# Performance work log

Measured on AMD Instinct MI355X. Metric: run time of the kernel, lower is better.

Reference implementation:

```python
import jax, jax.numpy as jnp
import numpy as np

SR = 44100.0
MIN_GAIN, MAX_GAIN = -48.0, 12.0
MIN_EQ, MAX_EQ = -15.0, 15.0
MIN_CTS, MAX_CTS = -20.0, 10.0
# Freeverb (JUCE Reverb, as used by pedalboard.Reverb) tunings @ 44.1 kHz
COMB_T = [1116, 1188, 1277, 1356, 1422, 1491, 1557, 1617]
AP_T = [556, 441, 341, 225]
COMB_OFF = [0]
for _L in COMB_T:
    COMB_OFF.append(COMB_OFF[-1] + _L)
AP_OFF = [0]
for _L in AP_T:
    AP_OFF.append(AP_OFF[-1] + _L)


def restore(x, lo, hi):
    # inverse of normalize-to-(0,1)
    return x * (hi - lo) + lo


def first_order(fc, kind):
    # bilinear-transform 1st-order HP/LP (pedalboard High/LowpassFilter are 1st order)
    K = jnp.tan(np.pi * fc / SR)
    a1 = (K - 1.0) / (K + 1.0)
    z = jnp.zeros_like(fc)
    if kind == "hp":
        b0 = 1.0 / (1.0 + K)
        b = jnp.stack([b0, -b0, z], -1)
    else:
        b0 = K / (1.0 + K)
        b = jnp.stack([b0, b0, z], -1)
    a = jnp.stack([jnp.ones_like(fc), a1, z], -1)
    return b, a


def shelf(fc, gain_db, high):
    # RBJ cookbook shelf, Q = 1/sqrt(2)
    A = 10.0 ** (gain_db / 40.0)
    w = 2.0 * np.pi * fc / SR
    cw = jnp.cos(w)
    alpha = jnp.sin(w) * (np.sqrt(2.0) / 2.0)
    sq = 2.0 * jnp.sqrt(A) * alpha
    s = 1.0 if high else -1.0
    b0 = A * ((A + 1.0) + s * (A - 1.0) * cw + sq)
    b1 = -2.0 * s * A * ((A - 1.0) + s * (A + 1.0) * cw)
    b2 = A * ((A + 1.0) + s * (A - 1.0) * cw - sq)
    a0 = (A + 1.0) - s * (A - 1.0) * cw + sq
    a1 = 2.0 * s * ((A - 1.0) - s * (A + 1.0) * cw)
    a2 = (A + 1.0) - s * (A - 1.0) * cw - sq
    return jnp.stack([b0, b1, b2], -1), jnp.stack([a0, a1, a2], -1)


def peak(fc, gain_db, q):
    # RBJ cookbook peaking EQ
    A = 10.0 ** (gain_db / 40.0)
    w = 2.0 * np.pi * fc / SR
    cw = jnp.cos(w)
    alpha = jnp.sin(w) / (2.0 * q)
    b = jnp.stack([1.0 + alpha * A, -2.0 * cw, 1.0 - alpha * A], -1)
    a = jnp.stack([1.0 + alpha / A, -2.0 * cw, 1.0 - alpha / A], -1)
    return b, a


def cascade_biquads(x, B, A):
    # x: [N, T]; B, A: [N, 6, 3]. DF2T cascade of 6 sections via one scan.
    B = B / A[..., :1]
    A = A / A[..., :1]
    n_sec = B.shape[1]

    def step(z, xt):  # z: [N, 6, 2], xt: [N]
        s = xt
        zn = []
        for k in range(n_sec):
            y = B[:, k, 0] * s + z[:, k, 0]
            z1 = B[:, k, 1] * s - A[:, k, 1] * y + z[:, k, 1]
            z2 = B[:, k, 2] * s - A[:, k, 2] * y
            zn.append(jnp.stack([z1, z2], -1))
            s = y
        return jnp.stack(zn, 1), s

    z0 = jnp.zeros((x.shape[0], n_sec, 2), x.dtype)
    _, y = jax.lax.scan(step, z0, x.T)
    return y.T


def compressor(x, thr_db, ratio, att_ms, rel_ms):
    # feed-forward compressor, dB-domain gain computer + one-pole attack/release
    a_att = jnp.exp(-1.0 / (att_ms * 1e-3 * SR))  # [N]
    a_rel = jnp.exp(-1.0 / (rel_ms * 1e-3 * SR))
    lvl = 20.0 * jnp.log10(jnp.abs(x) + 1e-6)  # [N, T]
    tgt = jnp.minimum(0.0, (thr_db[:, None] - lvl) * (1.0 - 1.0 / ratio[:, None]))

    def step(g, t):  # g, t: [N] gain reduction in dB (<= 0)
        coef = jnp.where(t < g, a_att, a_rel)
        g = coef * g + (1.0 - coef) * t
        return g, g

    _, g = jax.lax.scan(step, jnp.zeros(x.shape[0], x.dtype), tgt.T)
    return x * 10.0 ** (g.T / 20.0)


def freeverb(x, room, damp01, wet, dry, width):
    # JUCE/Freeverb mono: 8 parallel damped combs -> 4 series allpasses
    fb = room * 0.28 + 0.7
    damp = damp01 * 0.4
    wet1 = 3.0 * wet * 0.5 * (1.0 + width)
    dryg = 2.0 * dry
    N = x.shape[0]
    CL, AL = COMB_OFF[-1], AP_OFF[-1]

    def step(carry, xt):
        cb, ab, st, t = carry
        inp = xt * 0.015
        acc = jnp.zeros_like(xt)
        st_new = []
        for k in range(8):
            idx = COMB_OFF[k] + t % COMB_T[k]
            out = cb[:, idx]
            s = out * (1.0 - damp) + st[:, k] * damp
            cb = cb.at[:, idx].set(inp + s * fb)
            st_new.append(s)
            acc = acc + out
        for k in range(4):
            idx = AP_OFF[k] + t % AP_T[k]
            buf = ab[:, idx]
            ab = ab.at[:, idx].set(acc + buf * 0.5)
            acc = buf - acc
        y = acc * wet1 + xt * dryg
        return (cb, ab, jnp.stack(st_new, 1), t + 1), y

    carry0 = (jnp.zeros((N, CL), x.dtype), jnp.zeros((N, AL), x.dtype),
              jnp.zeros((N, 8), x.dtype), jnp.int32(0))
    _, y = jax.lax.scan(step, carry0, x.T)
    return y.T


def _forward(x, p):
    bs, nt, T = x.shape
    N = bs * nt
    xf = x.reshape(N, T)
    pf = p.reshape(N, 24)

    gain_in = restore(pf[:, 0], MIN_GAIN, MAX_GAIN)
    xf = xf * (10.0 ** (gain_in / 20.0))[:, None]

    hp_fc = restore(pf[:, 1], 0.0, 350.0)
    lp_fc = restore(pf[:, 2], 3000.0, 22000.0)
    hs_fc = restore(pf[:, 3], 1500.0, 16000.0)
    hs_g = restore(pf[:, 4], MIN_EQ, MAX_EQ)
    ls_fc = restore(pf[:, 5], 30.0, 450.0)
    ls_g = restore(pf[:, 6], MIN_EQ, MAX_EQ)
    mh_fc = restore(pf[:, 7], 600.0, 7000.0)
    mh_g = restore(pf[:, 8], MIN_EQ, MAX_EQ)
    mh_q = restore(pf[:, 9], 0.5, 3.0)
    ml_fc = restore(pf[:, 10], 200.0, 2500.0)
    ml_g = restore(pf[:, 11], MIN_EQ, MAX_EQ)
    ml_q = restore(pf[:, 12], 0.5, 3.0)
    c_thr = restore(pf[:, 13], MIN_CTS, MAX_CTS)
    c_rat = restore(pf[:, 14], 1.0, 20.0)
    c_att = restore(pf[:, 15], 1.0, 30.0)
    c_rel = restore(pf[:, 16], 100.0, 4000.0)

    coefs = [first_order(hp_fc, "hp"), first_order(lp_fc, "lp"),
             shelf(hs_fc, hs_g, True), shelf(ls_fc, ls_g, False),
             peak(mh_fc, mh_g, mh_q), peak(ml_fc, ml_g, ml_q)]
    B = jnp.stack([c[0] for c in coefs], 1)  # [N, 6, 3]
    A = jnp.stack([c[1] for c in coefs], 1)
    xf = cascade_biquads(xf, B, A)
    xf = compressor(xf, c_thr, c_rat, c_att, c_rel)
    xf = freeverb(xf, pf[:, 17], pf[:, 18], pf[:, 19], pf[:, 20], pf[:, 21])

    gain_out = restore(pf[:, 22], MIN_GAIN, MAX_GAIN)
    xf = xf * (10.0 ** (gain_out / 20.0))[:, None]

    pan = restore(pf[:, 23], 0.3, 0.7)
    theta = pan * (np.pi / 2.0)
    pang = jnp.stack([jnp.cos(theta), jnp.sin(theta)], -1).reshape(bs, nt, 2)
    y = jnp.einsum("bnt,bnc->bct", xf.reshape(bs, nt, T), pang)

    p_out = jnp.stack([gain_in, hp_fc, lp_fc, hs_fc, hs_g, ls_fc, ls_g,
                       mh_fc, mh_g, mh_q, ml_fc, ml_g, ml_q,
                       c_thr, c_rat, c_att, c_rel,
                       pf[:, 17], pf[:, 18], pf[:, 19], pf[:, 20], pf[:, 21],
                       gain_out, pan], -1).reshape(bs, nt, 24)
    return y, p_out


_forward_jit = jax.jit(_forward)


def setup_inputs() -> dict:
    key = jax.random.key(0)
    k1, k2 = jax.random.split(key)
    x = 0.1 * jax.random.normal(k1, (4, 8, 65536), dtype=jnp.float32)
    p = jax.random.uniform(k2, (4, 8, 24), dtype=jnp.float32)
    return {"x": x, "p": p}


def reference(x, p):
    return _forward_jit(x, p)
```

## Files before the change

kernel.cpp:

```cpp
#include <hip/hip_runtime.h>
#include <math.h>

#define T 65536
#define NCH 32
#define LCHUNK 512
#define CCHUNK 128
#define SB 256
#define NBLK 256
#define VH 8

#define OFS_A  0
#define OFS_B1 2097152
#define OFS_I  4194304
#define OFS_P  7340032
#define OFS_M  7342080
#define OFS_V  7346688
#define OFS_Z  7395840


__device__ void norm_store(double b0,double b1,double b2,double a0,double a1,double a2,
                           double* B, double* A1, double* A2, int k){
  B[k*3+0]=b0/a0; B[k*3+1]=b1/a0; B[k*3+2]=b2/a0; A1[k]=a1/a0; A2[k]=a2/a0;
}

__device__ void shelf_coefs(double fc, double g, double s, double* B, double* A1, double* A2, int k){
  double A  = pow(10.0, g/40.0);
  double w  = 2.0*3.14159265358979323846*fc/44100.0;
  double cw = cos(w);
  double al = sin(w)*0.70710678118654752;
  double sq = 2.0*sqrt(A)*al;
  double b0 = A*((A+1.0) + s*(A-1.0)*cw + sq);
  double b1 = -2.0*s*A*((A-1.0) + s*(A+1.0)*cw);
  double b2 = A*((A+1.0) + s*(A-1.0)*cw - sq);
  double a0 = (A+1.0) - s*(A-1.0)*cw + sq;
  double a1 = 2.0*s*((A-1.0) - s*(A+1.0)*cw);
  double a2 = (A+1.0) - s*(A-1.0)*cw - sq;
  norm_store(b0,b1,b2,a0,a1,a2,B,A1,A2,k);
}

__device__ void peak_coefs(double fc, double g, double q, double* B, double* A1, double* A2, int k){
  double A  = pow(10.0, g/40.0);
  double w  = 2.0*3.14159265358979323846*fc/44100.0;
  double cw = cos(w);
  double al = sin(w)/(2.0*q);
  norm_store(1.0+al*A, -2.0*cw, 1.0-al*A, 1.0+al/A, -2.0*cw, 1.0-al/A, B,A1,A2,k);
}

__global__ void k_params(const float* __restrict__ p, float* __restrict__ ws, float* __restrict__ pout){
  int ch = threadIdx.x;
  if (ch >= NCH) return;
  const float* pf = p + ch*24;
  float f[24];
  #pragma unroll
  for (int j=0;j<24;j++) f[j]=pf[j];

  double gain_in = (double)f[0]*60.0 - 48.0;
  double hp_fc  = (double)f[1]*350.0;
  double lp_fc  = (double)f[2]*19000.0 + 3000.0;
  double hs_fc  = (double)f[3]*14500.0 + 1500.0;
  double hs_g   = (double)f[4]*30.0 - 15.0;
  double ls_fc  = (double)f[5]*420.0 + 30.0;
  double ls_g   = (double)f[6]*30.0 - 15.0;
  double mh_fc  = (double)f[7]*6400.0 + 600.0;
  double mh_g   = (double)f[8]*30.0 - 15.0;
  double mh_q   = (double)f[9]*2.5 + 0.5;
  double ml_fc  = (double)f[10]*2300.0 + 200.0;
  double ml_g   = (double)f[11]*30.0 - 15.0;
  double ml_q   = (double)f[12]*2.5 + 0.5;
  double c_thr  = (double)f[13]*30.0 - 20.0;
  double c_rat  = (double)f[14]*19.0 + 1.0;
  double c_att  = (double)f[15]*29.0 + 1.0;
  double c_rel  = (double)f[16]*3900.0 + 100.0;
  double gain_out=(double)f[22]*60.0 - 48.0;
  double pan    = (double)f[23]*0.4 + 0.3;

  double B[18], A1[6], A2[6];
  { double K = tan(3.14159265358979323846*hp_fc/44100.0);
    double a1=(K-1.0)/(K+1.0), b0=1.0/(1.0+K);
    B[0]=b0; B[1]=-b0; B[2]=0.0; A1[0]=a1; A2[0]=0.0; }
  { double K = tan(3.14159265358979323846*lp_fc/44100.0);
    double a1=(K-1.0)/(K+1.0), b0=K/(1.0+K);
    B[3]=b0; B[4]=b0; B[5]=0.0; A1[1]=a1; A2[1]=0.0; }
  shelf_coefs(hs_fc, hs_g,  1.0, B, A1, A2, 2);
  shelf_coefs(ls_fc, ls_g, -1.0, B, A1, A2, 3);
  peak_coefs (mh_fc, mh_g, mh_q, B, A1, A2, 4);
  peak_coefs (ml_fc, ml_g, ml_q, B, A1, A2, 5);

  double gin = pow(10.0, gain_in/20.0);
  B[0]*=gin; B[1]*=gin; B[2]*=gin;

  float* Pc = ws + OFS_P + ch*64;
  #pragma unroll
  for (int k=0;k<6;k++){
    Pc[k]    = (float)B[k*3+0];
    Pc[6+k]  = (float)B[k*3+1];
    Pc[12+k] = (float)B[k*3+2];
    Pc[18+k] = (float)A1[k];
    Pc[24+k] = (float)A2[k];
  }
  Pc[30] = (float)c_thr;
  Pc[31] = (float)(1.0 - 1.0/c_rat);
  Pc[32] = (float)exp(-1.0/(c_att*0.001*44100.0));
  Pc[33] = (float)exp(-1.0/(c_rel*0.001*44100.0));
  double fb   = (double)f[17]*0.28 + 0.7;
  double damp = (double)f[18]*0.4;
  double wet1 = 3.0*(double)f[19]*0.5*(1.0+(double)f[21]);
  double dryg = 2.0*(double)f[20];
  double gout = pow(10.0, gain_out/20.0);
  Pc[34] = (float)fb;
  Pc[35] = (float)damp;
  Pc[36] = (float)(wet1*gout);
  Pc[37] = (float)(dryg*gout/0.015);
  Pc[38] = (float)cos(pan*1.57079632679489662);
  Pc[39] = (float)sin(pan*1.57079632679489662);

  float* po = pout + ch*24;
  po[0]=(float)gain_in; po[1]=(float)hp_fc; po[2]=(float)lp_fc; po[3]=(float)hs_fc;
  po[4]=(float)hs_g; po[5]=(float)ls_fc; po[6]=(float)ls_g; po[7]=(float)mh_fc;
  po[8]=(float)mh_g; po[9]=(float)mh_q; po[10]=(float)ml_fc; po[11]=(float)ml_g;
  po[12]=(float)ml_q; po[13]=(float)c_thr; po[14]=(float)c_rat; po[15]=(float)c_att;
  po[16]=(float)c_rel; po[17]=f[17]; po[18]=f[18]; po[19]=f[19]; po[20]=f[20];
  po[21]=f[21]; po[22]=(float)gain_out; po[23]=(float)pan;
}


__device__ __forceinline__ float bq_step(const float* b0, const float* b1, const float* b2,
                                         const float* a1, const float* a2,
                                         float* z1, float* z2, float s){
  #pragma unroll
  for (int k=0;k<6;k++){
    float y = fmaf(b0[k], s, z1[k]);
    z1[k] = fmaf(b1[k], s, fmaf(-a1[k], y, z2[k]));
    z2[k] = fmaf(b2[k], s, -a2[k]*y);
    s = y;
  }
  return s;
}

__device__ __forceinline__ void load_coefs(const float* Pc, float* b0, float* b1, float* b2,
                                           float* a1, float* a2){
  #pragma unroll
  for (int k=0;k<6;k++){
    b0[k]=Pc[k]; b1[k]=Pc[6+k]; b2[k]=Pc[12+k]; a1[k]=Pc[18+k]; a2[k]=Pc[24+k];
  }
}

__global__ __launch_bounds__(64,1) void k_chunk1(const float* __restrict__ x, float* __restrict__ ws){
  int tg = blockIdx.x*64 + threadIdx.x;
  int ch = tg / 140, sub = tg % 140;
  if (ch >= NCH) return;
  const float* Pc = ws + OFS_P + ch*64;
  float b0[6],b1[6],b2[6],a1[6],a2[6];
  load_coefs(Pc,b0,b1,b2,a1,a2);
  float z1[6]={0,0,0,0,0,0}, z2[6]={0,0,0,0,0,0};

  if (sub < CCHUNK){
    const float4* xp = (const float4*)(x + ch*T + sub*LCHUNK);
    for (int j=0;j<LCHUNK/4;j++){
      float4 v = xp[j];
      bq_step(b0,b1,b2,a1,a2,z1,z2,v.x);
      bq_step(b0,b1,b2,a1,a2,z1,z2,v.y);
      bq_step(b0,b1,b2,a1,a2,z1,z2,v.z);
      bq_step(b0,b1,b2,a1,a2,z1,z2,v.w);
    }
    float* vo = ws + OFS_V + (ch*CCHUNK + sub)*12;
    #pragma unroll
    for (int k=0;k<6;k++){ vo[2*k]=z1[k]; vo[2*k+1]=z2[k]; }
  } else {
    int j = sub - CCHUNK;
    if ((j & 1)==0) z1[j>>1]=1.0f; else z2[j>>1]=1.0f;
    for (int t=0;t<LCHUNK;t++) bq_step(b0,b1,b2,a1,a2,z1,z2,0.0f);
    float* mo = ws + OFS_M + ch*144 + j*12;
    #pragma unroll
    for (int k=0;k<6;k++){ mo[2*k]=z1[k]; mo[2*k+1]=z2[k]; }
  }
}

__global__ __launch_bounds__(64,1) void k_chunk2(float* __restrict__ ws){
  int ch = threadIdx.x;
  if (ch >= NCH) return;
  const float* M = ws + OFS_M + ch*144;
  const float* V = ws + OFS_V + ch*CCHUNK*12;
  float*       Z = ws + OFS_Z + ch*CCHUNK*12;
  float Mr[144];
  #pragma unroll
  for (int i=0;i<144;i++) Mr[i]=M[i];
  float z[12], vbuf[12];
  #pragma unroll
  for (int i=0;i<12;i++) z[i]=0.0f;
  #pragma unroll
  for (int i=0;i<12;i++) vbuf[i]=V[i];
  for (int c=0;c<CCHUNK;c++){
    #pragma unroll
    for (int i=0;i<12;i++) Z[c*12+i]=z[i];
    float zn[12];
    #pragma unroll
    for (int i=0;i<12;i++) zn[i]=vbuf[i];
    if (c+1<CCHUNK){
      #pragma unroll
      for (int i=0;i<12;i++) vbuf[i]=V[(c+1)*12+i];
    }
    #pragma unroll
    for (int j=0;j<12;j++){
      float zj = z[j];
      #pragma unroll
      for (int i=0;i<12;i++) zn[i] = fmaf(Mr[j*12+i], zj, zn[i]);
    }
    #pragma unroll
    for (int i=0;i<12;i++) z[i]=zn[i];
  }
}

__global__ __launch_bounds__(64,1) void k_chunk3(const float* __restrict__ x, float* __restrict__ ws){
  int tg = blockIdx.x*64 + threadIdx.x;
  int ch = tg >> 7, c = tg & (CCHUNK-1);
  const float* Pc = ws + OFS_P + ch*64;
  float b0[6],b1[6],b2[6],a1[6],a2[6];
  load_coefs(Pc,b0,b1,b2,a1,a2);
  float thr = Pc[30], rt = Pc[31];
  float aA = Pc[32], aR = Pc[33];
  float kA = 1.0f - aA, kR = 1.0f - aR;
  const float* Zi = ws + OFS_Z + (ch*CCHUNK + c)*12;
  float z1[6], z2[6];
  #pragma unroll
  for (int k=0;k<6;k++){ z1[k]=Zi[2*k]; z2[k]=Zi[2*k+1]; }
  const float4* xp = (const float4*)(x + ch*T + c*LCHUNK);
  float4* Ao  = (float4*)(ws + OFS_A  + (size_t)ch*T + c*LCHUNK);
  float4* B1o = (float4*)(ws + OFS_B1 + (size_t)ch*T + c*LCHUNK);
  float*  Ig  = ws + OFS_I + (size_t)ch*98304;

  for (int gg=0; gg<64; gg++){
    float4 v0 = xp[2*gg], v1 = xp[2*gg+1];
    float ya[8], Tv[8];
    ya[0]=bq_step(b0,b1,b2,a1,a2,z1,z2,v0.x);
    ya[1]=bq_step(b0,b1,b2,a1,a2,z1,z2,v0.y);
    ya[2]=bq_step(b0,b1,b2,a1,a2,z1,z2,v0.z);
    ya[3]=bq_step(b0,b1,b2,a1,a2,z1,z2,v0.w);
    ya[4]=bq_step(b0,b1,b2,a1,a2,z1,z2,v1.x);
    ya[5]=bq_step(b0,b1,b2,a1,a2,z1,z2,v1.y);
    ya[6]=bq_step(b0,b1,b2,a1,a2,z1,z2,v1.z);
    ya[7]=bq_step(b0,b1,b2,a1,a2,z1,z2,v1.w);
    #pragma unroll
    for (int s=0;s<8;s++)
      Tv[s] = fminf(0.0f, (thr - 6.0205999132796239f*log2f(fabsf(ya[s])+1e-6f))*rt);
    Ao[2*gg]   = make_float4(ya[0],ya[1],ya[2],ya[3]);
    Ao[2*gg+1] = make_float4(ya[4],ya[5],ya[6],ya[7]);
    B1o[2*gg]   = make_float4(Tv[0],Tv[1],Tv[2],Tv[3]);
    B1o[2*gg+1] = make_float4(Tv[4],Tv[5],Tv[6],Tv[7]);
    float bb[9];
    bb[0] = kR*Tv[0]; bb[1] = kA*Tv[0];
    #pragma unroll
    for (int s=1;s<8;s++){
      float bA = kA*Tv[s], bR = kR*Tv[s];
      bb[s+1] = fmaf(aA, bb[s], bA);
      #pragma unroll
      for (int j=7;j>=1;j--){
        if (j<=s) bb[j] = fminf(fmaf(aA, bb[j-1], bA), fmaf(aR, bb[j], bR));
      }
      bb[0] = fmaf(aR, bb[0], bR);
    }
    int G = c*64 + gg;
    float* ig = Ig + (G>>5)*384 + (G&31)*12;
    *(float4*)(ig)   = make_float4(bb[0],bb[1],bb[2],bb[3]);
    *(float4*)(ig+4) = make_float4(bb[4],bb[5],bb[6],bb[7]);
    *(float4*)(ig+8) = make_float4(bb[8],0.0f,0.0f,0.0f);
  }
}


__global__ __launch_bounds__(320) void k_verb(float* __restrict__ ws){
  const int LC[8] = {1116,1188,1277,1356,1422,1491,1557,1617};
  const int COFF[8] = {0,1116,2304,3581,4937,6359,7850,9407};
  const int LA[4] = {556,441,341,225};
  const int AOFF[4] = {0,556,997,1338};
  int ch = blockIdx.x, tid = threadIdx.x;
  __shared__ float cb[11024];
  __shared__ float ab[1563];
  __shared__ float cH[8][264];
  __shared__ float xts[256];
  __shared__ float B1st[2][256];
  __shared__ float IldS[384];
  __shared__ float gB[2][32];
  __shared__ float xfer[32];
  const float* Pc = ws + OFS_P + ch*64;
  float fb = Pc[34], damp = Pc[35], wet1 = Pc[36], dryk = Pc[37];
  float aA = Pc[32], aR = Pc[33];
  float kA = 1.0f - aA, kR = 1.0f - aR;
  float omd = 1.0f - damp;
  float* Aio = ws + OFS_A + (size_t)ch*T;
  const float* B1c = ws + OFS_B1 + (size_t)ch*T;
  const float* IG  = ws + OFS_I + (size_t)ch*98304;
  for (int i=tid;i<11024;i+=320) cb[i]=0.0f;
  for (int i=tid;i<1563;i+=320)  ab[i]=0.0f;
  for (int i=tid;i<8*264;i+=320) ((float*)cH)[i]=0.0f;
  bool scanw = (tid >= 256);
  int sl = tid - 256;
  float w[VH];
  { float pw = 1.0f;
    #pragma unroll
    for (int d=0;d<VH;d++){ w[d]=pw; pw*=damp; } }
  float sj[9];
  { float pA = 1.0f;
    #pragma unroll
    for (int j=0;j<9;j++){ sj[j]=pA; pA*=aA; }
    float pR = 1.0f;
    #pragma unroll
    for (int j=8;j>=0;j--){ sj[j]*=pR; pR*=aR; } }
  int cbb[8] = {0,0,0,0,0,0,0,0};
  int abb[4] = {0,0,0,0};
  float gcarry = 0.0f;
  float4 iR0, iR1, bR;
  float xv = 0.0f;

  if (scanw){
    const float4* isrc = (const float4*)(IG);
    float4* idst = (float4*)IldS;
    idst[sl] = isrc[sl];
    if (sl < 32) idst[64+sl] = isrc[64+sl];
    iR0 = isrc[96+sl];
    if (sl < 32) iR1 = isrc[96+64+sl];
    const float4* bsrc = (const float4*)(B1c);
    ((float4*)B1st[0])[sl] = bsrc[sl];
    ((float4*)B1st[1])[sl] = bsrc[64+sl];
  }
  if (tid < 256) xv = Aio[tid];
  __syncthreads();
  if (tid == 256){
    float g = 0.0f;
    for (int m=0;m<32;m++){
      gB[0][m] = g;
      const float* Ip = &IldS[m*12];
      float f0=fmaf(sj[0],g,Ip[0]), f1=fmaf(sj[1],g,Ip[1]), f2=fmaf(sj[2],g,Ip[2]);
      float f3=fmaf(sj[3],g,Ip[3]), f4=fmaf(sj[4],g,Ip[4]), f5=fmaf(sj[5],g,Ip[5]);
      float f6=fmaf(sj[6],g,Ip[6]), f7=fmaf(sj[7],g,Ip[7]), f8=fmaf(sj[8],g,Ip[8]);
      g = fminf(fminf(fminf(f0,f1),fminf(f2,f3)),
                fminf(fminf(f4,f5),fminf(fminf(f6,f7),f8)));
    }
    gcarry = g;
  }
  __syncthreads();

  for (int i=0;i<NBLK;i++){
    int t0 = i<<8;
    int p = i & 1;
    float xt = 0.0f, acc = 0.0f, a = 0.0f;
    int idx1=0, idx2=0, idx3=0, idx4=0;
    float bv1=0.f, bv2=0.f, bv3=0.f, bv4=0.f;
    if (tid < 256){
      int m = tid>>3, r = tid&7;
      float g = gB[p][m];
      const float* Bl = B1st[p] + (m<<3);
      float4 q0 = *(const float4*)(Bl);
      float4 q1 = *(const float4*)(Bl+4);
      float tv[8] = {q0.x,q0.y,q0.z,q0.w,q1.x,q1.y,q1.z,q1.w};
      #pragma unroll
      for (int s=0;s<8;s++){
        if (s<=r){
          float tt = tv[s];
          g = fminf(fmaf(aA,g,kA*tt), fmaf(aR,g,kR*tt));
        }
      }
      xt = xv * exp2f(g*0.16609640474436813f) * 0.015f;
      xts[tid] = xt;
      #pragma unroll
      for (int k=0;k<8;k++){
        int idx = cbb[k]+tid; if (idx>=LC[k]) idx-=LC[k];
        float o = cb[COFF[k]+idx];
        cH[k][VH+tid] = omd*o;
        acc += o;
      }
      idx1 = abb[0]+tid; if (idx1>=LA[0]) idx1-=LA[0];
      idx2 = abb[1]+tid; if (idx2>=LA[1]) idx2-=LA[1];
      idx3 = abb[2]+tid; if (idx3>=LA[2]) idx3-=LA[2];
      bv1 = ab[AOFF[0]+idx1];
      bv2 = ab[AOFF[1]+idx2];
      bv3 = ab[AOFF[2]+idx3];
    } else if (i+1 < NBLK){
      float4* idst = (float4*)IldS;
      idst[sl] = iR0;
      if (sl < 32) idst[64+sl] = iR1;
      if (i >= 1) ((float4*)B1st[(i+1)&1])[sl] = bR;
    }
    __syncthreads();
    if (tid < 256){
      if (i+1 < NBLK) xv = Aio[t0+256+tid];
      #pragma unroll
      for (int k=0;k<8;k++){
        float s = 0.0f;
        #pragma unroll
        for (int d=0;d<VH;d++) s = fmaf(w[d], cH[k][VH+tid-d], s);
        int idx = cbb[k]+tid; if (idx>=LC[k]) idx-=LC[k];
        cb[COFF[k]+idx] = fmaf(fb, s, xt);
      }
      a = acc;
      ab[AOFF[0]+idx1] = fmaf(0.5f, bv1, a); a = bv1 - a;
      ab[AOFF[1]+idx2] = fmaf(0.5f, bv2, a); a = bv2 - a;
      ab[AOFF[2]+idx3] = fmaf(0.5f, bv3, a); a = bv3 - a;
      if (tid >= 225) xfer[tid-225] = a;
      idx4 = abb[3]+tid; if (idx4>=225) idx4-=225; if (idx4>=225) idx4-=225;
      if (tid < 225) bv4 = ab[AOFF[3]+idx4];
    } else {
      if (i+2 < NBLK){
        const float4* isrc = (const float4*)(IG + (size_t)(i+2)*384);
        iR0 = isrc[sl];
        if (sl < 32) iR1 = isrc[64+sl];
        const float4* bsrc = (const float4*)(B1c + (size_t)(i+2)*SB);
        bR = bsrc[sl];
      }
      if (tid == 256 && i+1 < NBLK){
        int q = (i+1)&1;
        float g = gcarry;
        #pragma unroll 4
        for (int m=0;m<32;m++){
          gB[q][m] = g;
          const float* Ip = &IldS[m*12];
          float f0=fmaf(sj[0],g,Ip[0]), f1=fmaf(sj[1],g,Ip[1]), f2=fmaf(sj[2],g,Ip[2]);
          float f3=fmaf(sj[3],g,Ip[3]), f4=fmaf(sj[4],g,Ip[4]), f5=fmaf(sj[5],g,Ip[5]);
          float f6=fmaf(sj[6],g,Ip[6]), f7=fmaf(sj[7],g,Ip[7]), f8=fmaf(sj[8],g,Ip[8]);
          g = fminf(fminf(fminf(f0,f1),fminf(f2,f3)),
                    fminf(fminf(f4,f5),fminf(fminf(f6,f7),f8)));
        }
        gcarry = g;
      }
    }
    __syncthreads();
    if (tid < 225){
      float bv = bv4;
      float b  = fmaf(0.5f, bv, a);
      float y  = bv - a;
      Aio[t0+tid] = fmaf(y, wet1, xts[tid]*dryk);
      if (tid < 31){
        float a2 = xfer[tid];
        float y2 = b - a2;
        ab[AOFF[3]+idx4] = fmaf(0.5f, b, a2);
        Aio[t0+225+tid] = fmaf(y2, wet1, xts[225+tid]*dryk);
      } else {
        ab[AOFF[3]+idx4] = b;
      }
    } else if (tid >= 232 && tid < 288){
      int q = tid-232; int k = q/7, d = q%7;
      cH[k][1+d] = cH[k][257+d];
    }
    #pragma unroll
    for (int k=0;k<8;k++){ cbb[k]+=SB; if (cbb[k]>=LC[k]) cbb[k]-=LC[k]; }
    #pragma unroll
    for (int j=0;j<4;j++){
      abb[j]+=SB;
      if (abb[j]>=LA[j]) abb[j]-=LA[j];
      if (abb[j]>=LA[j]) abb[j]-=LA[j];
    }
    __syncthreads();
  }
}


__global__ void k_mix(const float* __restrict__ ws, float* __restrict__ out){
  int id = blockIdx.x*256 + threadIdx.x;
  int t = id & (T-1), b = id >> 16;
  const float* Av = ws + OFS_A + (size_t)b*8*T + t;
  const float* P = ws + OFS_P;
  float s0=0.0f, s1=0.0f;
  #pragma unroll
  for (int n=0;n<8;n++){
    float v = Av[(size_t)n*T];
    int ch = b*8+n;
    s0 = fmaf(v, P[ch*64+38], s0);
    s1 = fmaf(v, P[ch*64+39], s1);
  }
  out[b*2*T + t]     = s0;
  out[b*2*T + T + t] = s1;
}

extern "C" void kernel_launch(void* const* d_in, const int* in_sizes, int n_in,
                              void* d_out, int out_size, void* d_ws, size_t ws_size,
                              hipStream_t stream) {
  const float* x = (const float*)d_in[0];
  const float* p = (const float*)d_in[1];
  float* out = (float*)d_out;
  float* ws  = (float*)d_ws;

  k_params<<<1, 64, 0, stream>>>(p, ws, out + 4*2*T);
  k_chunk1<<<70, 64, 0, stream>>>(x, ws);
  k_chunk2<<<1, 64, 0, stream>>>(ws);
  k_chunk3<<<64, 64, 0, stream>>>(x, ws);
  k_verb  <<<NCH, 320, 0, stream>>>(ws);
  k_mix   <<<(4*T)/256, 256, 0, stream>>>(ws, out);
}
```

Before: 911.9 us.

## Double reverb block size to 512 samples with deferred last allpass stage

The freeverb kernel now handles 512 samples per iteration with 576 threads instead of 256 with 320, halving the number of serial block iterations and barriers. Because allpass lengths are shorter than the block, the allpass stages are split across the two phases, and the 225-length final allpass plus output write are deferred into the next iteration, with an epilogue after the loop. The envelope-scan thread's per-block work is split into two halves placed in separate phases. It moves to dynamic shared memory of about 80 KB and sets the max-dynamic-smem attribute on every launch. This risks correctness at the allpass wraparound boundaries and adds per-iteration work for the single scan thread.

```diff
diff --git a/kernel.cpp b/kernel.cpp
--- a/kernel.cpp
+++ b/kernel.cpp
@@ -5,8 +5,6 @@
 #define NCH 32
 #define LCHUNK 512
 #define CCHUNK 128
-#define SB 256
-#define NBLK 256
 #define VH 8
 
 #define OFS_A  0
@@ -268,20 +266,22 @@
 }
 
 
-__global__ __launch_bounds__(320) void k_verb(float* __restrict__ ws){
+__global__ __launch_bounds__(576) void k_verb(float* __restrict__ ws){
   const int LC[8] = {1116,1188,1277,1356,1422,1491,1557,1617};
   const int COFF[8] = {0,1116,2304,3581,4937,6359,7850,9407};
   const int LA[4] = {556,441,341,225};
   const int AOFF[4] = {0,556,997,1338};
+  const int SBV = 512, NBLKV = 128;
+  extern __shared__ float smem[];
+  float* cb    = smem;
+  float* ab    = smem + 11024;
+  float* cHf   = smem + 12588;
+  float* xtsD  = smem + 16748;
+  float* aLds  = smem + 17772;
+  float* B1stD = smem + 18284;
+  float* IldS  = smem + 19308;
+  float* gBD   = smem + 20076;
   int ch = blockIdx.x, tid = threadIdx.x;
-  __shared__ float cb[11024];
-  __shared__ float ab[1563];
-  __shared__ float cH[8][264];
-  __shared__ float xts[256];
-  __shared__ float B1st[2][256];
-  __shared__ float IldS[384];
-  __shared__ float gB[2][32];
-  __shared__ float xfer[32];
   const float* Pc = ws + OFS_P + ch*64;
   float fb = Pc[34], damp = Pc[35], wet1 = Pc[36], dryk = Pc[37];
   float aA = Pc[32], aR = Pc[33];
@@ -290,11 +290,9 @@
   float* Aio = ws + OFS_A + (size_t)ch*T;
   const float* B1c = ws + OFS_B1 + (size_t)ch*T;
   const float* IG  = ws + OFS_I + (size_t)ch*98304;
-  for (int i=tid;i<11024;i+=320) cb[i]=0.0f;
-  for (int i=tid;i<1563;i+=320)  ab[i]=0.0f;
-  for (int i=tid;i<8*264;i+=320) ((float*)cH)[i]=0.0f;
-  bool scanw = (tid >= 256);
-  int sl = tid - 256;
+  for (int i=tid;i<16748;i+=576) smem[i]=0.0f;
+  bool scanw = (tid >= 512);
+  int sl = tid - 512;
   float w[VH];
   { float pw = 1.0f;
     #pragma unroll
@@ -308,27 +306,32 @@
     for (int j=8;j>=0;j--){ sj[j]*=pR; pR*=aR; } }
   int cbb[8] = {0,0,0,0,0,0,0,0};
   int abb[4] = {0,0,0,0};
+  int ab4p = 0;
   float gcarry = 0.0f;
-  float4 iR0, iR1, bR;
+  float4 iR0, iR1, iR2, bR0, bR1;
   float xv = 0.0f;
 
   if (scanw){
     const float4* isrc = (const float4*)(IG);
     float4* idst = (float4*)IldS;
-    idst[sl] = isrc[sl];
-    if (sl < 32) idst[64+sl] = isrc[64+sl];
-    iR0 = isrc[96+sl];
-    if (sl < 32) iR1 = isrc[96+64+sl];
+    idst[sl]     = isrc[sl];
+    idst[64+sl]  = isrc[64+sl];
+    idst[128+sl] = isrc[128+sl];
+    const float4* i1 = (const float4*)(IG + 768);
+    iR0 = i1[sl]; iR1 = i1[64+sl]; iR2 = i1[128+sl];
     const float4* bsrc = (const float4*)(B1c);
-    ((float4*)B1st[0])[sl] = bsrc[sl];
-    ((float4*)B1st[1])[sl] = bsrc[64+sl];
-  }
-  if (tid < 256) xv = Aio[tid];
+    ((float4*)B1stD)[sl]        = bsrc[sl];
+    ((float4*)B1stD)[64+sl]     = bsrc[64+sl];
+    ((float4*)(B1stD+512))[sl]    = bsrc[128+sl];
+    ((float4*)(B1stD+512))[64+sl] = bsrc[192+sl];
+  } else {
+    xv = Aio[tid];
+  }
   __syncthreads();
-  if (tid == 256){
+  if (tid == 512){
     float g = 0.0f;
-    for (int m=0;m<32;m++){
-      gB[0][m] = g;
+    for (int m=0;m<64;m++){
+      gBD[m] = g;
       const float* Ip = &IldS[m*12];
       float f0=fmaf(sj[0],g,Ip[0]), f1=fmaf(sj[1],g,Ip[1]), f2=fmaf(sj[2],g,Ip[2]);
       float f3=fmaf(sj[3],g,Ip[3]), f4=fmaf(sj[4],g,Ip[4]), f5=fmaf(sj[5],g,Ip[5]);
@@ -340,16 +343,35 @@
   }
   __syncthreads();
 
-  for (int i=0;i<NBLK;i++){
-    int t0 = i<<8;
+  for (int i=0;i<NBLKV;i++){
+    int t0 = i<<9;
     int p = i & 1;
     float xt = 0.0f, acc = 0.0f, a = 0.0f;
-    int idx1=0, idx2=0, idx3=0, idx4=0;
-    float bv1=0.f, bv2=0.f, bv3=0.f, bv4=0.f;
-    if (tid < 256){
+    if (tid < 512){
+      if (i > 0 && tid < 225){
+        const float* xtsP = xtsD + (p^1)*512;
+        int slot = ab4p + tid; if (slot >= 225) slot -= 225;
+        float bv  = ab[AOFF[3]+slot];
+        float a0  = aLds[tid];
+        float y0  = bv - a0;
+        float v1  = fmaf(0.5f, bv, a0);
+        Aio[t0-512+tid] = fmaf(y0, wet1, xtsP[tid]*dryk);
+        float a1v = aLds[225+tid];
+        float y1  = v1 - a1v;
+        float v2  = fmaf(0.5f, v1, a1v);
+        Aio[t0-512+225+tid] = fmaf(y1, wet1, xtsP[225+tid]*dryk);
+        float vf = v2;
+        if (tid < 62){
+          float a2v = aLds[450+tid];
+          float y2  = v2 - a2v;
+          vf = fmaf(0.5f, v2, a2v);
+          Aio[t0-512+450+tid] = fmaf(y2, wet1, xtsP[450+tid]*dryk);
+        }
+        ab[AOFF[3]+slot] = vf;
+      }
       int m = tid>>3, r = tid&7;
-      float g = gB[p][m];
-      const float* Bl = B1st[p] + (m<<3);
+      float g = gBD[p*64+m];
+      const float* Bl = B1stD + p*512 + (m<<3);
       float4 q0 = *(const float4*)(Bl);
       float4 q1 = *(const float4*)(Bl+4);
       float tv[8] = {q0.x,q0.y,q0.z,q0.w,q1.x,q1.y,q1.z,q1.w};
@@ -361,58 +383,70 @@
         }
       }
       xt = xv * exp2f(g*0.16609640474436813f) * 0.015f;
-      xts[tid] = xt;
+      xtsD[p*512+tid] = xt;
       #pragma unroll
       for (int k=0;k<8;k++){
         int idx = cbb[k]+tid; if (idx>=LC[k]) idx-=LC[k];
         float o = cb[COFF[k]+idx];
-        cH[k][VH+tid] = omd*o;
+        cHf[k*520+VH+tid] = omd*o;
         acc += o;
       }
-      idx1 = abb[0]+tid; if (idx1>=LA[0]) idx1-=LA[0];
-      idx2 = abb[1]+tid; if (idx2>=LA[1]) idx2-=LA[1];
-      idx3 = abb[2]+tid; if (idx3>=LA[2]) idx3-=LA[2];
-      bv1 = ab[AOFF[0]+idx1];
-      bv2 = ab[AOFF[1]+idx2];
-      bv3 = ab[AOFF[2]+idx3];
-    } else if (i+1 < NBLK){
+    } else if (i+1 < NBLKV){
       float4* idst = (float4*)IldS;
-      idst[sl] = iR0;
-      if (sl < 32) idst[64+sl] = iR1;
-      if (i >= 1) ((float4*)B1st[(i+1)&1])[sl] = bR;
+      idst[sl]     = iR0;
+      idst[64+sl]  = iR1;
+      idst[128+sl] = iR2;
+      if (i >= 1){
+        float4* bdst = (float4*)(B1stD + ((i+1)&1)*512);
+        bdst[sl]    = bR0;
+        bdst[64+sl] = bR1;
+      }
     }
     __syncthreads();
-    if (tid < 256){
-      if (i+1 < NBLK) xv = Aio[t0+256+tid];
+    if (tid < 512){
+      if (i+1 < NBLKV) xv = Aio[t0+512+tid];
       #pragma unroll
       for (int k=0;k<8;k++){
         float s = 0.0f;
         #pragma unroll
-        for (int d=0;d<VH;d++) s = fmaf(w[d], cH[k][VH+tid-d], s);
+        for (int d=0;d<VH;d++) s = fmaf(w[d], cHf[k*520+VH+tid-d], s);
         int idx = cbb[k]+tid; if (idx>=LC[k]) idx-=LC[k];
         cb[COFF[k]+idx] = fmaf(fb, s, xt);
       }
       a = acc;
-      ab[AOFF[0]+idx1] = fmaf(0.5f, bv1, a); a = bv1 - a;
-      ab[AOFF[1]+idx2] = fmaf(0.5f, bv2, a); a = bv2 - a;
-      ab[AOFF[2]+idx3] = fmaf(0.5f, bv3, a); a = bv3 - a;
-      if (tid >= 225) xfer[tid-225] = a;
-      idx4 = abb[3]+tid; if (idx4>=225) idx4-=225; if (idx4>=225) idx4-=225;
-      if (tid < 225) bv4 = ab[AOFF[3]+idx4];
+      { int idx = abb[0]+tid;
+        if (idx>=LA[0]) idx-=LA[0]; if (idx>=LA[0]) idx-=LA[0]; if (idx>=LA[0]) idx-=LA[0];
+        float bv = ab[AOFF[0]+idx];
+        ab[AOFF[0]+idx] = fmaf(0.5f, bv, a);
+        a = bv - a; }
+      if (tid < 441){
+        int idx = abb[1]+tid;
+        if (idx>=LA[1]) idx-=LA[1]; if (idx>=LA[1]) idx-=LA[1]; if (idx>=LA[1]) idx-=LA[1];
+        float bv = ab[AOFF[1]+idx];
+        ab[AOFF[1]+idx] = fmaf(0.5f, bv, a);
+        a = bv - a;
+      }
+      if (tid < 341){
+        int idx = abb[2]+tid;
+        if (idx>=LA[2]) idx-=LA[2]; if (idx>=LA[2]) idx-=LA[2]; if (idx>=LA[2]) idx-=LA[2];
+        float bv = ab[AOFF[2]+idx];
+        ab[AOFF[2]+idx] = fmaf(0.5f, bv, a);
+        a = bv - a;
+        aLds[tid] = a;
+      }
     } else {
-      if (i+2 < NBLK){
-        const float4* isrc = (const float4*)(IG + (size_t)(i+2)*384);
-        iR0 = isrc[sl];
-        if (sl < 32) iR1 = isrc[64+sl];
-        const float4* bsrc = (const float4*)(B1c + (size_t)(i+2)*SB);
-        bR = bsrc[sl];
-      }
-      if (tid == 256 && i+1 < NBLK){
+      if (i+2 < NBLKV){
+        const float4* isrc = (const float4*)(IG + (size_t)(i+2)*768);
+        iR0 = isrc[sl]; iR1 = isrc[64+sl]; iR2 = isrc[128+sl];
+        const float4* bsrc = (const float4*)(B1c + (size_t)(i+2)*SBV);
+        bR0 = bsrc[sl]; bR1 = bsrc[64+sl];
+      }
+      if (tid == 512 && i+1 < NBLKV){
         int q = (i+1)&1;
         float g = gcarry;
         #pragma unroll 4
         for (int m=0;m<32;m++){
-          gB[q][m] = g;
+          gBD[q*64+m] = g;
           const float* Ip = &IldS[m*12];
           float f0=fmaf(sj[0],g,Ip[0]), f1=fmaf(sj[1],g,Ip[1]), f2=fmaf(sj[2],g,Ip[2]);
           float f3=fmaf(sj[3],g,Ip[3]), f4=fmaf(sj[4],g,Ip[4]), f5=fmaf(sj[5],g,Ip[5]);
@@ -424,32 +458,70 @@
       }
     }
     __syncthreads();
-    if (tid < 225){
-      float bv = bv4;
-      float b  = fmaf(0.5f, bv, a);
-      float y  = bv - a;
-      Aio[t0+tid] = fmaf(y, wet1, xts[tid]*dryk);
-      if (tid < 31){
-        float a2 = xfer[tid];
-        float y2 = b - a2;
-        ab[AOFF[3]+idx4] = fmaf(0.5f, b, a2);
-        Aio[t0+225+tid] = fmaf(y2, wet1, xts[225+tid]*dryk);
-      } else {
-        ab[AOFF[3]+idx4] = b;
-      }
-    } else if (tid >= 232 && tid < 288){
-      int q = tid-232; int k = q/7, d = q%7;
-      cH[k][1+d] = cH[k][257+d];
-    }
-    #pragma unroll
-    for (int k=0;k<8;k++){ cbb[k]+=SB; if (cbb[k]>=LC[k]) cbb[k]-=LC[k]; }
+    if (tid < 512){
+      if (tid >= 441){
+        int idx = abb[1]+tid;
+        if (idx>=LA[1]) idx-=LA[1]; if (idx>=LA[1]) idx-=LA[1]; if (idx>=LA[1]) idx-=LA[1];
+        float bv = ab[AOFF[1]+idx];
+        ab[AOFF[1]+idx] = fmaf(0.5f, bv, a);
+        a = bv - a;
+      }
+      if (tid >= 341){
+        int idx = abb[2]+tid;
+        if (idx>=LA[2]) idx-=LA[2]; if (idx>=LA[2]) idx-=LA[2]; if (idx>=LA[2]) idx-=LA[2];
+        float bv = ab[AOFF[2]+idx];
+        ab[AOFF[2]+idx] = fmaf(0.5f, bv, a);
+        a = bv - a;
+        aLds[tid] = a;
+      }
+      if (tid < 56){
+        int k = tid/7, d = tid%7;
+        cHf[k*520+1+d] = cHf[k*520+513+d];
+      }
+    } else {
+      if (tid == 512 && i+1 < NBLKV){
+        int q = (i+1)&1;
+        float g = gcarry;
+        #pragma unroll 4
+        for (int m=32;m<64;m++){
+          gBD[q*64+m] = g;
+          const float* Ip = &IldS[m*12];
+          float f0=fmaf(sj[0],g,Ip[0]), f1=fmaf(sj[1],g,Ip[1]), f2=fmaf(sj[2],g,Ip[2]);
+          float f3=fmaf(sj[3],g,Ip[3]), f4=fmaf(sj[4],g,Ip[4]), f5=fmaf(sj[5],g,Ip[5]);
+          float f6=fmaf(sj[6],g,Ip[6]), f7=fmaf(sj[7],g,Ip[7]), f8=fmaf(sj[8],g,Ip[8]);
+          g = fminf(fminf(fminf(f0,f1),fminf(f2,f3)),
+                    fminf(fminf(f4,f5),fminf(fminf(f6,f7),f8)));
+        }
+        gcarry = g;
+      }
+    }
+    ab4p = abb[3];
+    #pragma unroll
+    for (int k=0;k<8;k++){ cbb[k]+=SBV; if (cbb[k]>=LC[k]) cbb[k]-=LC[k]; }
     #pragma unroll
     for (int j=0;j<4;j++){
-      abb[j]+=SB;
+      abb[j]+=SBV;
       if (abb[j]>=LA[j]) abb[j]-=LA[j];
       if (abb[j]>=LA[j]) abb[j]-=LA[j];
+      if (abb[j]>=LA[j]) abb[j]-=LA[j];
     }
     __syncthreads();
+  }
+  if (tid < 225){
+    int t0e = (NBLKV-1)<<9;
+    const float* xtsP = xtsD + ((NBLKV-1)&1)*512;
+    int slot = ab4p + tid; if (slot >= 225) slot -= 225;
+    float bv  = ab[AOFF[3]+slot];
+    float a0  = aLds[tid];
+    float v1  = fmaf(0.5f, bv, a0);
+    Aio[t0e+tid] = fmaf(bv - a0, wet1, xtsP[tid]*dryk);
+    float a1v = aLds[225+tid];
+    float v2  = fmaf(0.5f, v1, a1v);
+    Aio[t0e+225+tid] = fmaf(v1 - a1v, wet1, xtsP[225+tid]*dryk);
+    if (tid < 62){
+      float a2v = aLds[450+tid];
+      Aio[t0e+450+tid] = fmaf(v2 - a2v, wet1, xtsP[450+tid]*dryk);
+    }
   }
 }
 
@@ -479,10 +551,13 @@
   float* out = (float*)d_out;
   float* ws  = (float*)d_ws;
 
+  (void)hipFuncSetAttribute((const void*)k_verb,
+                            hipFuncAttributeMaxDynamicSharedMemorySize, 131072);
+
   k_params<<<1, 64, 0, stream>>>(p, ws, out + 4*2*T);
   k_chunk1<<<70, 64, 0, stream>>>(x, ws);
   k_chunk2<<<1, 64, 0, stream>>>(ws);
   k_chunk3<<<64, 64, 0, stream>>>(x, ws);
-  k_verb  <<<NCH, 320, 0, stream>>>(ws);
+  k_verb  <<<NCH, 576, 20204*4, stream>>>(ws);
   k_mix   <<<(4*T)/256, 256, 0, stream>>>(ws, out);
 }
```

Measured after the change: 1.325 ms. 45.3% more time.
